# Optimization experiments

Hardware: AMD Instinct MI355X
Metric: run time of the kernel (lower is better)

The kernel has to match this reference:

```python
import jax, jax.numpy as jnp
import numpy as np

N_USER = 500_000
N_GROUP = 100_000
N_EDGE = 5_000_000
DIM = 64
NORM_2 = -1.0  # exponent for back-pass degree norm (module default)
ALPHA = 0.0    # residual mix coefficient (module default)


def setup_inputs() -> dict:
    key = jax.random.key(0)
    k1, k2, k3, k4 = jax.random.split(key, 4)
    h_user = jax.random.normal(k1, (N_USER, DIM), dtype=jnp.float32)
    h_group = jax.random.normal(k2, (N_GROUP, DIM), dtype=jnp.float32)
    edge_src = jax.random.randint(k3, (N_EDGE,), 0, N_USER, dtype=jnp.int64)
    edge_dst = jax.random.randint(k4, (N_EDGE,), 0, N_GROUP, dtype=jnp.int64)
    return {"h_user": h_user, "h_group": h_group,
            "edge_src": edge_src, "edge_dst": edge_dst}


def reference(h_user, h_group, edge_src, edge_dst):
    # Forward pass: copy_src -> sum aggregate onto dst, normalize by in-degree^-1.
    ones = jnp.ones((edge_src.shape[0],), dtype=h_user.dtype)
    deg_dst = jax.ops.segment_sum(ones, edge_dst, num_segments=N_GROUP)
    deg_dst = jnp.maximum(deg_dst, 1.0)  # clamp(min=1)
    rst = jax.ops.segment_sum(h_user[edge_src], edge_dst, num_segments=N_GROUP)
    if ALPHA != 0.0:
        rst = rst + ALPHA * h_group
    rst = rst * (1.0 / deg_dst)[:, None]  # [N_GROUP, DIM]
    # Back pass: aggregate rst back onto src via reversed edges, normalize by deg^norm_2.
    deg_src = jax.ops.segment_sum(ones, edge_src, num_segments=N_USER)
    deg_src = jnp.maximum(deg_src, 1.0)
    bsrc = jax.ops.segment_sum(rst[edge_dst], edge_src, num_segments=N_USER)
    bsrc = bsrc * jnp.power(deg_src, NORM_2)[:, None]  # [N_USER, DIM]
    return bsrc, rst
```

## Files before the change

### kernel.cpp

```cpp
#include <hip/hip_runtime.h>

#define N_USER  500000
#define N_GROUP 100000
#define N_EDGE  5000000
#define DIM     64

#define SCAN_BLOCK 256
#define SCAN_ELEMS 4096
#define PER_THREAD (SCAN_ELEMS / SCAN_BLOCK)

#define KD_SHIFT 7
#define KS_SHIFT 9
#define C_DST ((N_GROUP + (1 << KD_SHIFT) - 1) >> KD_SHIFT)
#define C_SRC ((N_USER  + (1 << KS_SHIFT) - 1) >> KS_SHIFT)
#define TILE_A 16384
#define GRID_A ((N_EDGE + TILE_A - 1) / TILE_A)
#define CVT_BLOCKS 1024
#define CAP_D 7680
#define CAP_S 6272
#define MD_N (C_DST * GRID_A)
#define MS_N (C_SRC * GRID_A)

typedef unsigned int uint32;

__device__ inline unsigned short f2bf(float x) {
    uint32 b = __float_as_uint(x);
    uint32 r = (b + 0x7FFFu + ((b >> 16) & 1u)) >> 16;
    return (unsigned short)r;
}
__device__ inline float ldt(const float* t, size_t i) { return t[i]; }
__device__ inline float ldt(const unsigned short* t, size_t i) {
    return __uint_as_float((uint32)t[i] << 16);
}

__global__ void prep_kernel(const int* __restrict__ src,
                            const int* __restrict__ dst,
                            int* __restrict__ mat_d,
                            int* __restrict__ mat_s,
                            const float* __restrict__ hin,
                            unsigned short* __restrict__ h16) {
    __shared__ int hd[C_DST], hs[C_SRC];
    int tid = threadIdx.x;
    int b = blockIdx.x;
    if (b < GRID_A) {
        long base = (long)b * TILE_A;
        for (int k = tid; k < C_DST; k += blockDim.x) hd[k] = 0;
        for (int k = tid; k < C_SRC; k += blockDim.x) hs[k] = 0;
        __syncthreads();
        for (int i = tid; i < TILE_A; i += blockDim.x) {
            long e = base + i;
            if (e >= N_EDGE) break;
            atomicAdd(&hd[dst[e] >> KD_SHIFT], 1);
            atomicAdd(&hs[src[e] >> KS_SHIFT], 1);
        }
        __syncthreads();
        for (int k = tid; k < C_DST; k += blockDim.x) mat_d[(size_t)k * GRID_A + b] = hd[k];
        for (int k = tid; k < C_SRC; k += blockDim.x) mat_s[(size_t)k * GRID_A + b] = hs[k];
    } else if (h16) {
        long n4 = (long)N_USER * DIM / 4;
        long stride = (long)CVT_BLOCKS * blockDim.x;
        for (long i = (long)(b - GRID_A) * blockDim.x + tid; i < n4; i += stride) {
            const float4 v = ((const float4*)hin)[i];
            ushort4 o;
            o.x = f2bf(v.x); o.y = f2bf(v.y); o.z = f2bf(v.z); o.w = f2bf(v.w);
            ((ushort4*)h16)[i] = o;
        }
    }
}

__global__ void scan1_kernel(const int* __restrict__ cnt,
                             int* __restrict__ off,
                             int* __restrict__ partial,
                             int n) {
    __shared__ int sh[SCAN_BLOCK];
    int tid = threadIdx.x;
    int tbase = blockIdx.x * SCAN_ELEMS + tid * PER_THREAD;
    int local[PER_THREAD];
    int sum = 0;
#pragma unroll
    for (int i = 0; i < PER_THREAD; ++i) {
        int idx = tbase + i;
        int v = (idx < n) ? cnt[idx] : 0;
        local[i] = sum;
        sum += v;
    }
    sh[tid] = sum;
    __syncthreads();
    for (int o = 1; o < SCAN_BLOCK; o <<= 1) {
        int t = (tid >= o) ? sh[tid - o] : 0;
        __syncthreads();
        sh[tid] += t;
        __syncthreads();
    }
    int texc = sh[tid] - sum;
    int blockTotal = sh[SCAN_BLOCK - 1];
#pragma unroll
    for (int i = 0; i < PER_THREAD; ++i) {
        int idx = tbase + i;
        if (idx < n) off[idx] = local[i] + texc;
    }
    if (tid == 0) partial[blockIdx.x] = blockTotal;
}

__global__ void scan2_kernel(int* __restrict__ partial, int nb,
                             int* __restrict__ off_end) {
    __shared__ int sh[SCAN_BLOCK];
    int tid = threadIdx.x;
    int v = (tid < nb) ? partial[tid] : 0;
    sh[tid] = v;
    __syncthreads();
    for (int o = 1; o < SCAN_BLOCK; o <<= 1) {
        int t = (tid >= o) ? sh[tid - o] : 0;
        __syncthreads();
        sh[tid] += t;
        __syncthreads();
    }
    if (tid < nb) partial[tid] = sh[tid] - v;
    if (tid == 0) *off_end = sh[SCAN_BLOCK - 1];
}

__global__ void scan3_kernel(int* __restrict__ off,
                             const int* __restrict__ partial, int n) {
    int base = blockIdx.x * SCAN_ELEMS;
    int add = partial[blockIdx.x];
    for (int i = threadIdx.x; i < SCAN_ELEMS; i += blockDim.x) {
        int idx = base + i;
        if (idx < n) off[idx] += add;
    }
}

__global__ void passA(const int* __restrict__ src,
                      const int* __restrict__ dst,
                      const int* __restrict__ mat_d,
                      const int* __restrict__ mat_s,
                      uint32* __restrict__ coarse_dst,
                      uint32* __restrict__ coarse_src) {
    __shared__ int bd[C_DST], bs[C_SRC];
    int tid = threadIdx.x;
    int b = blockIdx.x;
    long base = (long)b * TILE_A;

    for (int c = tid; c < C_DST; c += blockDim.x) bd[c] = mat_d[(size_t)c * GRID_A + b];
    for (int c = tid; c < C_SRC; c += blockDim.x) bs[c] = mat_s[(size_t)c * GRID_A + b];
    __syncthreads();

    for (int i = tid; i < TILE_A; i += blockDim.x) {
        long e = base + i;
        if (e >= N_EDGE) break;
        int g = dst[e], u = src[e];
        int cd = g >> KD_SHIFT;
        int pd = atomicAdd(&bd[cd], 1);
        coarse_dst[pd] = ((uint32)(g & ((1 << KD_SHIFT) - 1)) << 20) | (uint32)u;
        int cs = u >> KS_SHIFT;
        int ps = atomicAdd(&bs[cs], 1);
        coarse_src[ps] = ((uint32)(u & ((1 << KS_SHIFT) - 1)) << 20) | (uint32)g;
    }
}

template <int SHIFT, int CAP, int U, bool NT, typename T>
__global__ __launch_bounds__(512) void sortgather(
    const uint32* __restrict__ coarse,
    const int* __restrict__ mat,
    const T* __restrict__ table,
    float* __restrict__ out,
    unsigned short* __restrict__ p0,
    unsigned short* __restrict__ p1,
    int n) {
    const int NK = 1 << SHIFT;
    __shared__ int vals[CAP];
    __shared__ int hist[NK];
    __shared__ int cur[NK];
    int tid = threadIdx.x;
    int c = blockIdx.x;
    int lo_g = c << SHIFT;
    int beg = mat[(size_t)c * GRID_A];
    int end = mat[(size_t)(c + 1) * GRID_A];
    int cnt = end - beg;
    int stg = min(cnt, CAP);

    for (int k = tid; k < NK; k += 512) hist[k] = 0;
    __syncthreads();

    for (int i = tid; i < stg; i += 512) {
        atomicAdd(&hist[coarse[beg + i] >> 20], 1);
    }
    __syncthreads();

    for (int o = 1; o < NK; o <<= 1) {
        int t = (tid < NK && tid >= o) ? hist[tid - o] : 0;
        __syncthreads();
        if (tid < NK) hist[tid] += t;
        __syncthreads();
    }
    if (tid < NK) cur[tid] = (tid == 0) ? 0 : hist[tid - 1];
    __syncthreads();

    for (int i = tid; i < stg; i += 512) {
        uint32 kv = coarse[beg + i];
        int p = atomicAdd(&cur[kv >> 20], 1);
        vals[p] = (int)(kv & 0xFFFFFu);
    }
    __syncthreads();

    int wv = tid >> 6, lane = tid & 63;
    for (int r = wv; r < NK; r += 8) {
        int row = lo_g + r;
        if (row >= n) break;
        int lo = (r == 0) ? 0 : hist[r - 1];
        int hi = hist[r];
        float a[U];
#pragma unroll
        for (int j = 0; j < U; ++j) a[j] = 0.0f;
        int e = lo;
        for (; e + U <= hi; e += U) {
#pragma unroll
            for (int j = 0; j < U; ++j) {
                int s = vals[e + j];
                a[j] += ldt(table, (size_t)s * DIM + lane);
            }
        }
        for (; e < hi; ++e) {
            int s = vals[e];
            a[0] += ldt(table, (size_t)s * DIM + lane);
        }
        int deg = hi - lo;
        if (stg < cnt) {
            for (int i = beg + stg; i < end; ++i) {
                uint32 kv = coarse[i];
                if ((int)(kv >> 20) == r) {
                    a[0] += ldt(table, (size_t)(kv & 0xFFFFFu) * DIM + lane);
                    ++deg;
                }
            }
        }
        float acc = 0.0f;
#pragma unroll
        for (int j = 0; j < U; ++j) acc += a[j];
        float rv = acc / fmaxf((float)deg, 1.0f);
        size_t oidx = (size_t)row * DIM + lane;
        if (NT) __builtin_nontemporal_store(rv, &out[oidx]);
        else out[oidx] = rv;
        if (p0) {
            unsigned short bv = f2bf(rv);
            if (lane < 32) p0[(size_t)row * 32 + lane] = bv;
            else           p1[(size_t)row * 32 + (lane - 32)] = bv;
        }
    }
}

template <int SHIFT, int CAP>
__global__ __launch_bounds__(512) void sortgather_bwd(
    const uint32* __restrict__ coarse,
    const int* __restrict__ mat,
    const unsigned short* __restrict__ p0,
    const unsigned short* __restrict__ p1,
    float* __restrict__ out,
    int n) {
    const int NK = 1 << SHIFT;
    __shared__ int vals[CAP];
    __shared__ int hist[NK];
    __shared__ int cur[NK];
    int tid = threadIdx.x;
    int c = blockIdx.x;
    int lo_g = c << SHIFT;
    int beg = mat[(size_t)c * GRID_A];
    int end = mat[(size_t)(c + 1) * GRID_A];
    int cnt = end - beg;
    int stg = min(cnt, CAP);

    for (int k = tid; k < NK; k += 512) hist[k] = 0;
    __syncthreads();
    for (int i = tid; i < stg; i += 512) {
        atomicAdd(&hist[coarse[beg + i] >> 20], 1);
    }
    __syncthreads();
    for (int o = 1; o < NK; o <<= 1) {
        int t = (tid < NK && tid >= o) ? hist[tid - o] : 0;
        __syncthreads();
        if (tid < NK) hist[tid] += t;
        __syncthreads();
    }
    if (tid < NK) cur[tid] = (tid == 0) ? 0 : hist[tid - 1];
    __syncthreads();
    for (int i = tid; i < stg; i += 512) {
        uint32 kv = coarse[beg + i];
        int p = atomicAdd(&cur[kv >> 20], 1);
        vals[p] = (int)(kv & 0xFFFFFu);
    }
    __syncthreads();

    int wv = tid >> 6, lane = tid & 63;
    int sub = lane >> 5, d = lane & 31;
    for (int h = 0; h < 2; ++h) {
        const unsigned short* pl = h ? p1 : p0;
        for (int r = wv; r < NK; r += 8) {
            int row = lo_g + r;
            if (row >= n) break;
            int lo = (r == 0) ? 0 : hist[r - 1];
            int hi = hist[r];
            int deg = hi - lo;
            float a = 0.0f, b2 = 0.0f;
            int e = lo;
            for (; e + 4 <= hi; e += 4) {
                int s0 = vals[e + sub];
                int s1 = vals[e + 2 + sub];
                a  += ldt(pl, (size_t)s0 * 32 + d);
                b2 += ldt(pl, (size_t)s1 * 32 + d);
            }
            for (; e < hi; e += 2) {
                int ee = e + sub;
                float w = (ee < hi) ? 1.0f : 0.0f;
                int s = vals[ee < hi ? ee : hi - 1];
                a += w * ldt(pl, (size_t)s * 32 + d);
            }
            if (stg < cnt) {
                for (int i = beg + stg; i < end; ++i) {
                    uint32 kv = coarse[i];
                    if ((int)(kv >> 20) == r) {
                        float w = (sub == 0) ? 1.0f : 0.0f;
                        a += w * ldt(pl, (size_t)(kv & 0xFFFFFu) * 32 + d);
                        ++deg;
                    }
                }
            }
            float s = a + b2;
            s += __shfl_xor(s, 32);
            float rv = s / fmaxf((float)deg, 1.0f);
            if (sub == 0)
                __builtin_nontemporal_store(rv, &out[(size_t)row * DIM + h * 32 + d]);
        }
    }
}

__global__ void hist_kernel(const int* __restrict__ src,
                            const int* __restrict__ dst,
                            int* __restrict__ cnt_src,
                            int* __restrict__ cnt_dst) {
    int e = blockIdx.x * blockDim.x + threadIdx.x;
    if (e < N_EDGE) {
        atomicAdd(&cnt_src[src[e]], 1);
        atomicAdd(&cnt_dst[dst[e]], 1);
    }
}

__global__ void fill_both(const int* __restrict__ src,
                          const int* __restrict__ dst,
                          const int* __restrict__ off_src,
                          const int* __restrict__ off_dst,
                          int* __restrict__ cur_src,
                          int* __restrict__ cur_dst,
                          int* __restrict__ bucket_src,
                          int* __restrict__ bucket_dst) {
    int e = blockIdx.x * blockDim.x + threadIdx.x;
    if (e < N_EDGE) {
        int u = src[e];
        int g = dst[e];
        int p = atomicAdd(&cur_src[u], 1);
        bucket_src[off_src[u] + p] = g;
        int q = atomicAdd(&cur_dst[g], 1);
        bucket_dst[off_dst[g] + q] = u;
    }
}

__global__ void fill_one(const int* __restrict__ key,
                         const int* __restrict__ val,
                         const int* __restrict__ off,
                         int* __restrict__ cur,
                         int* __restrict__ bucket) {
    int e = blockIdx.x * blockDim.x + threadIdx.x;
    if (e < N_EDGE) {
        int k = key[e];
        int p = atomicAdd(&cur[k], 1);
        bucket[off[k] + p] = val[e];
    }
}

__global__ void cvt_bf16(const float* __restrict__ in,
                         unsigned short* __restrict__ out, long n4) {
    long i = (long)blockIdx.x * blockDim.x + threadIdx.x;
    if (i >= n4) return;
    const float4 v = ((const float4*)in)[i];
    ushort4 o;
    o.x = f2bf(v.x); o.y = f2bf(v.y); o.z = f2bf(v.z); o.w = f2bf(v.w);
    ((ushort4*)out)[i] = o;
}

template <int NROW, bool NT, int U, typename T>
__global__ void gather_kernel(const int* __restrict__ off,
                              const int* __restrict__ bucket,
                              const T* __restrict__ table,
                              float* __restrict__ out,
                              unsigned short* __restrict__ out16) {
    int wid = (blockIdx.x * blockDim.x + threadIdx.x) >> 6;
    int lane = threadIdx.x & 63;
    if (wid >= NROW) return;
    int beg = off[wid], end = off[wid + 1];

    float a[U];
#pragma unroll
    for (int j = 0; j < U; ++j) a[j] = 0.0f;

    for (int b = beg; b < end; b += 64) {
        int navail = min(64, end - b);
        int sv = bucket[b + (lane < navail ? lane : 0)];
        int k = 0;
        for (; k + U <= navail; k += U) {
#pragma unroll
            for (int j = 0; j < U; ++j) {
                int s = __shfl(sv, k + j);
                a[j] += ldt(table, (size_t)s * DIM + lane);
            }
        }
        if (k < navail) {
#pragma unroll
            for (int j = 0; j < U; ++j) {
                int kk = k + j;
                int s = __shfl(sv, kk < navail ? kk : navail - 1);
                float w = (kk < navail) ? 1.0f : 0.0f;
                a[j] += w * ldt(table, (size_t)s * DIM + lane);
            }
        }
    }
    float acc = 0.0f;
#pragma unroll
    for (int j = 0; j < U; ++j) acc += a[j];
    float inv = 1.0f / fmaxf((float)(end - beg), 1.0f);
    float r = acc * inv;
    if (NT) {
        __builtin_nontemporal_store(r, &out[(size_t)wid * DIM + lane]);
    } else {
        out[(size_t)wid * DIM + lane] = r;
    }
    if (out16) out16[(size_t)wid * DIM + lane] = f2bf(r);
}

__global__ void deg_kernel(const int* __restrict__ src,
                           const int* __restrict__ dst,
                           float* __restrict__ deg_src,
                           float* __restrict__ deg_dst) {
    int e = blockIdx.x * blockDim.x + threadIdx.x;
    if (e < N_EDGE) {
        unsafeAtomicAdd(&deg_src[src[e]], 1.0f);
        unsafeAtomicAdd(&deg_dst[dst[e]], 1.0f);
    }
}

__global__ void scatter_fwd(const int* __restrict__ src,
                            const int* __restrict__ dst,
                            const float* __restrict__ h_user,
                            float* __restrict__ rst) {
    long idx = (long)blockIdx.x * blockDim.x + threadIdx.x;
    if (idx >= (long)N_EDGE * DIM) return;
    int e = (int)(idx >> 6), d = (int)(idx & 63);
    unsafeAtomicAdd(&rst[(long)dst[e] * DIM + d], h_user[(long)src[e] * DIM + d]);
}

__global__ void norm_kernel(float* __restrict__ x,
                            const float* __restrict__ deg, long total) {
    long idx = (long)blockIdx.x * blockDim.x + threadIdx.x;
    if (idx >= total) return;
    float dg = fmaxf(deg[idx >> 6], 1.0f);
    x[idx] *= (1.0f / dg);
}

__global__ void scatter_bwd(const int* __restrict__ src,
                            const int* __restrict__ dst,
                            const float* __restrict__ rst,
                            float* __restrict__ bsrc) {
    long idx = (long)blockIdx.x * blockDim.x + threadIdx.x;
    if (idx >= (long)N_EDGE * DIM) return;
    int e = (int)(idx >> 6), d = (int)(idx & 63);
    unsafeAtomicAdd(&bsrc[(long)src[e] * DIM + d], rst[(long)dst[e] * DIM + d]);
}

extern "C" void kernel_launch(void* const* d_in, const int* in_sizes, int n_in,
                              void* d_out, int out_size, void* d_ws, size_t ws_size,
                              hipStream_t stream) {
    const float* h_user   = (const float*)d_in[0];
    const int*   edge_src = (const int*)d_in[2];
    const int*   edge_dst = (const int*)d_in[3];

    float* bsrc = (float*)d_out;
    float* rst  = bsrc + (size_t)N_USER * DIM;

    const int BLK = 256;
    const int grid_e = (N_EDGE + BLK - 1) / BLK;

    int* ws      = (int*)d_ws;
    int* cnt_dst = ws;
    int* off_dst = cnt_dst + N_GROUP;
    int* cnt_src = off_dst + N_GROUP + 1;
    int* off_src = cnt_src + N_USER;
    int* cur_dst = off_src + N_USER + 1;
    int* cur_src = cur_dst + N_GROUP;
    int* partial = cur_src + N_USER;
    int* bucket_dst = partial + 256;
    int* bucket_src = bucket_dst + N_EDGE;
    unsigned short* r16 = (unsigned short*)(bucket_src + N_EDGE);
    unsigned short* h16 = r16 + (size_t)N_GROUP * DIM;
    unsigned short* rp0 = r16;
    unsigned short* rp1 = r16 + (size_t)N_GROUP * 32;
    size_t tail = ((size_t)((char*)(h16 + (size_t)N_USER * DIM) - (char*)d_ws) + 7) & ~(size_t)7;
    int* mat_d = (int*)((char*)d_ws + tail);
    int* mat_s = mat_d + MD_N + 1;
    size_t tail2 = ((size_t)((char*)(mat_s + MS_N + 1) - (char*)d_ws) + 7) & ~(size_t)7;
    uint32* coarse_dst = (uint32*)((char*)d_ws + tail2);
    uint32* coarse_src = coarse_dst + N_EDGE;

    size_t need_csr1 = (size_t)((bucket_dst + N_EDGE) - ws) * sizeof(int);
    size_t need_csr2 = (size_t)((bucket_src + N_EDGE) - ws) * sizeof(int);
    size_t need_r16  = need_csr2 + (size_t)N_GROUP * DIM * 2;
    size_t need_full = need_r16 + (size_t)N_USER * DIM * 2;
    size_t need_ms   = (size_t)((char*)(coarse_src + N_EDGE) - (char*)d_ws);

    int nb_dst = (N_GROUP + SCAN_ELEMS - 1) / SCAN_ELEMS;
    int nb_src = (N_USER + SCAN_ELEMS - 1) / SCAN_ELEMS;

    if (ws_size >= need_ms) {
        bool use_h16 = (ws_size >= need_full);
        bool use_r16 = (ws_size >= need_r16);

        int gridP = GRID_A + (use_h16 ? CVT_BLOCKS : 0);
        prep_kernel<<<gridP, BLK, 0, stream>>>(edge_src, edge_dst, mat_d, mat_s,
                                               h_user, use_h16 ? h16 : nullptr);

        int nb_md = (MD_N + SCAN_ELEMS - 1) / SCAN_ELEMS;
        int nb_ms = (MS_N + SCAN_ELEMS - 1) / SCAN_ELEMS;
        scan1_kernel<<<nb_md, SCAN_BLOCK, 0, stream>>>(mat_d, mat_d, partial, MD_N);
        scan2_kernel<<<1, SCAN_BLOCK, 0, stream>>>(partial, nb_md, mat_d + MD_N);
        scan3_kernel<<<nb_md, SCAN_BLOCK, 0, stream>>>(mat_d, partial, MD_N);
        scan1_kernel<<<nb_ms, SCAN_BLOCK, 0, stream>>>(mat_s, mat_s, partial, MS_N);
        scan2_kernel<<<1, SCAN_BLOCK, 0, stream>>>(partial, nb_ms, mat_s + MS_N);
        scan3_kernel<<<nb_ms, SCAN_BLOCK, 0, stream>>>(mat_s, partial, MS_N);

        passA<<<GRID_A, BLK, 0, stream>>>(edge_src, edge_dst, mat_d, mat_s,
                                          coarse_dst, coarse_src);

        if (use_h16) {
            sortgather<KD_SHIFT, CAP_D, 8, false, unsigned short>
                <<<C_DST, 512, 0, stream>>>(coarse_dst, mat_d, h16, rst,
                                            use_r16 ? rp0 : nullptr,
                                            use_r16 ? rp1 : nullptr, N_GROUP);
        } else {
            sortgather<KD_SHIFT, CAP_D, 8, false, float>
                <<<C_DST, 512, 0, stream>>>(coarse_dst, mat_d, h_user, rst,
                                            use_r16 ? rp0 : nullptr,
                                            use_r16 ? rp1 : nullptr, N_GROUP);
        }
        if (use_r16) {
            sortgather_bwd<KS_SHIFT, CAP_S>
                <<<C_SRC, 512, 0, stream>>>(coarse_src, mat_s, rp0, rp1, bsrc, N_USER);
        } else {
            sortgather<KS_SHIFT, CAP_S, 4, true, float>
                <<<C_SRC, 512, 0, stream>>>(coarse_src, mat_s, rst, bsrc,
                                            nullptr, nullptr, N_USER);
        }
        return;
    }

    if (ws_size >= need_csr2) {
        bool use_h16 = (ws_size >= need_full);
        bool use_r16 = (ws_size >= need_r16);

        hipMemsetAsync(d_ws, 0, (size_t)(partial - ws) * sizeof(int), stream);

        if (use_h16) {
            long n4 = (long)N_USER * DIM / 4;
            cvt_bf16<<<(int)((n4 + BLK - 1) / BLK), BLK, 0, stream>>>(h_user, h16, n4);
        }

        hist_kernel<<<grid_e, BLK, 0, stream>>>(edge_src, edge_dst, cnt_src, cnt_dst);

        scan1_kernel<<<nb_dst, SCAN_BLOCK, 0, stream>>>(cnt_dst, off_dst, partial, N_GROUP);
        scan2_kernel<<<1, SCAN_BLOCK, 0, stream>>>(partial, nb_dst, off_dst + N_GROUP);
        scan3_kernel<<<nb_dst, SCAN_BLOCK, 0, stream>>>(off_dst, partial, N_GROUP);

        scan1_kernel<<<nb_src, SCAN_BLOCK, 0, stream>>>(cnt_src, off_src, partial, N_USER);
        scan2_kernel<<<1, SCAN_BLOCK, 0, stream>>>(partial, nb_src, off_src + N_USER);
        scan3_kernel<<<nb_src, SCAN_BLOCK, 0, stream>>>(off_src, partial, N_USER);

        fill_both<<<grid_e, BLK, 0, stream>>>(
            edge_src, edge_dst, off_src, off_dst,
            cur_src, cur_dst, bucket_src, bucket_dst);

        unsigned short* r16p = use_r16 ? r16 : (unsigned short*)nullptr;
        if (use_h16) {
            gather_kernel<N_GROUP, false, 8, unsigned short>
                <<<(N_GROUP * 64 + BLK - 1) / BLK, BLK, 0, stream>>>(
                    off_dst, bucket_dst, h16, rst, r16p);
        } else {
            gather_kernel<N_GROUP, false, 8, float>
                <<<(N_GROUP * 64 + BLK - 1) / BLK, BLK, 0, stream>>>(
                    off_dst, bucket_dst, h_user, rst, r16p);
        }
        if (use_r16) {
            gather_kernel<N_USER, true, 4, unsigned short>
                <<<(int)(((size_t)N_USER * 64 + BLK - 1) / BLK), BLK, 0, stream>>>(
                    off_src, bucket_src, r16, bsrc, nullptr);
        } else {
            gather_kernel<N_USER, true, 4, float>
                <<<(int)(((size_t)N_USER * 64 + BLK - 1) / BLK), BLK, 0, stream>>>(
                    off_src, bucket_src, rst, bsrc, nullptr);
        }
        return;
    }

    if (ws_size >= need_csr1) {
        hipMemsetAsync(d_ws, 0, (size_t)(partial - ws) * sizeof(int), stream);
        hist_kernel<<<grid_e, BLK, 0, stream>>>(edge_src, edge_dst, cnt_src, cnt_dst);

        scan1_kernel<<<nb_dst, SCAN_BLOCK, 0, stream>>>(cnt_dst, off_dst, partial, N_GROUP);
        scan2_kernel<<<1, SCAN_BLOCK, 0, stream>>>(partial, nb_dst, off_dst + N_GROUP);
        scan3_kernel<<<nb_dst, SCAN_BLOCK, 0, stream>>>(off_dst, partial, N_GROUP);

        scan1_kernel<<<nb_src, SCAN_BLOCK, 0, stream>>>(cnt_src, off_src, partial, N_USER);
        scan2_kernel<<<1, SCAN_BLOCK, 0, stream>>>(partial, nb_src, off_src + N_USER);
        scan3_kernel<<<nb_src, SCAN_BLOCK, 0, stream>>>(off_src, partial, N_USER);

        fill_one<<<grid_e, BLK, 0, stream>>>(edge_dst, edge_src, off_dst, cur_dst, bucket_dst);
        gather_kernel<N_GROUP, false, 8, float>
            <<<(N_GROUP * 64 + BLK - 1) / BLK, BLK, 0, stream>>>(
                off_dst, bucket_dst, h_user, rst, nullptr);

        fill_one<<<grid_e, BLK, 0, stream>>>(edge_src, edge_dst, off_src, cur_src, bucket_dst);
        gather_kernel<N_USER, true, 4, float>
            <<<(int)(((size_t)N_USER * 64 + BLK - 1) / BLK), BLK, 0, stream>>>(
                off_src, bucket_dst, rst, bsrc, nullptr);
        return;
    }

    float* deg_dst = (float*)d_ws;
    float* deg_src = deg_dst + N_GROUP;
    hipMemsetAsync(d_out, 0, (size_t)(N_USER + N_GROUP) * DIM * sizeof(float), stream);
    hipMemsetAsync(d_ws, 0, (size_t)(N_USER + N_GROUP) * sizeof(float), stream);

    deg_kernel<<<grid_e, BLK, 0, stream>>>(edge_src, edge_dst, deg_src, deg_dst);

    long total_ed = (long)N_EDGE * DIM;
    int grid_ed = (int)((total_ed + BLK - 1) / BLK);
    scatter_fwd<<<grid_ed, BLK, 0, stream>>>(edge_src, edge_dst, h_user, rst);
    long total_g = (long)N_GROUP * DIM;
    norm_kernel<<<(int)((total_g + BLK - 1) / BLK), BLK, 0, stream>>>(rst, deg_dst, total_g);
    scatter_bwd<<<grid_ed, BLK, 0, stream>>>(edge_src, edge_dst, rst, bsrc);
    long total_u = (long)N_USER * DIM;
    norm_kernel<<<(int)((total_u + BLK - 1) / BLK), BLK, 0, stream>>>(bsrc, deg_src, total_u);
}
```

Before: 634.6 us.

## Merge dst/src bucket scans into one and drop split-half bf16 backward gather

Lays the dst and src bucket-count matrices out contiguously so a single three-kernel scan produces offsets for both, writing into one shared coarse buffer. This removes three kernel launches. It also stores the bf16 copy of rst as full 64-wide rows instead of two 32-column halves. The backward pass then reuses the generic sortgather kernel (bf16 table, 4-way unroll) in place of the specialized half-row kernel. The change trades the half-split layout's smaller per-pass working set for fewer passes over the edge lists and simpler row gathers.

```diff
diff --git a/kernel.cpp b/kernel.cpp
--- a/kernel.cpp
+++ b/kernel.cpp
@@ -20,6 +20,7 @@
 #define CAP_S 6272
 #define MD_N (C_DST * GRID_A)
 #define MS_N (C_SRC * GRID_A)
+#define MC_N (MD_N + MS_N)
 
 typedef unsigned int uint32;
 
@@ -133,8 +134,7 @@
                       const int* __restrict__ dst,
                       const int* __restrict__ mat_d,
                       const int* __restrict__ mat_s,
-                      uint32* __restrict__ coarse_dst,
-                      uint32* __restrict__ coarse_src) {
+                      uint32* __restrict__ coarse) {
     __shared__ int bd[C_DST], bs[C_SRC];
     int tid = threadIdx.x;
     int b = blockIdx.x;
@@ -150,10 +150,10 @@
         int g = dst[e], u = src[e];
         int cd = g >> KD_SHIFT;
         int pd = atomicAdd(&bd[cd], 1);
-        coarse_dst[pd] = ((uint32)(g & ((1 << KD_SHIFT) - 1)) << 20) | (uint32)u;
+        coarse[pd] = ((uint32)(g & ((1 << KD_SHIFT) - 1)) << 20) | (uint32)u;
         int cs = u >> KS_SHIFT;
         int ps = atomicAdd(&bs[cs], 1);
-        coarse_src[ps] = ((uint32)(u & ((1 << KS_SHIFT) - 1)) << 20) | (uint32)g;
+        coarse[ps] = ((uint32)(u & ((1 << KS_SHIFT) - 1)) << 20) | (uint32)g;
     }
 }
 
@@ -163,8 +163,7 @@
     const int* __restrict__ mat,
     const T* __restrict__ table,
     float* __restrict__ out,
-    unsigned short* __restrict__ p0,
-    unsigned short* __restrict__ p1,
+    unsigned short* __restrict__ out16,
     int n) {
     const int NK = 1 << SHIFT;
     __shared__ int vals[CAP];
@@ -240,95 +239,7 @@
         size_t oidx = (size_t)row * DIM + lane;
         if (NT) __builtin_nontemporal_store(rv, &out[oidx]);
         else out[oidx] = rv;
-        if (p0) {
-            unsigned short bv = f2bf(rv);
-            if (lane < 32) p0[(size_t)row * 32 + lane] = bv;
-            else           p1[(size_t)row * 32 + (lane - 32)] = bv;
-        }
-    }
-}
-
-template <int SHIFT, int CAP>
-__global__ __launch_bounds__(512) void sortgather_bwd(
-    const uint32* __restrict__ coarse,
-    const int* __restrict__ mat,
-    const unsigned short* __restrict__ p0,
-    const unsigned short* __restrict__ p1,
-    float* __restrict__ out,
-    int n) {
-    const int NK = 1 << SHIFT;
-    __shared__ int vals[CAP];
-    __shared__ int hist[NK];
-    __shared__ int cur[NK];
-    int tid = threadIdx.x;
-    int c = blockIdx.x;
-    int lo_g = c << SHIFT;
-    int beg = mat[(size_t)c * GRID_A];
-    int end = mat[(size_t)(c + 1) * GRID_A];
-    int cnt = end - beg;
-    int stg = min(cnt, CAP);
-
-    for (int k = tid; k < NK; k += 512) hist[k] = 0;
-    __syncthreads();
-    for (int i = tid; i < stg; i += 512) {
-        atomicAdd(&hist[coarse[beg + i] >> 20], 1);
-    }
-    __syncthreads();
-    for (int o = 1; o < NK; o <<= 1) {
-        int t = (tid < NK && tid >= o) ? hist[tid - o] : 0;
-        __syncthreads();
-        if (tid < NK) hist[tid] += t;
-        __syncthreads();
-    }
-    if (tid < NK) cur[tid] = (tid == 0) ? 0 : hist[tid - 1];
-    __syncthreads();
-    for (int i = tid; i < stg; i += 512) {
-        uint32 kv = coarse[beg + i];
-        int p = atomicAdd(&cur[kv >> 20], 1);
-        vals[p] = (int)(kv & 0xFFFFFu);
-    }
-    __syncthreads();
-
-    int wv = tid >> 6, lane = tid & 63;
-    int sub = lane >> 5, d = lane & 31;
-    for (int h = 0; h < 2; ++h) {
-        const unsigned short* pl = h ? p1 : p0;
-        for (int r = wv; r < NK; r += 8) {
-            int row = lo_g + r;
-            if (row >= n) break;
-            int lo = (r == 0) ? 0 : hist[r - 1];
-            int hi = hist[r];
-            int deg = hi - lo;
-            float a = 0.0f, b2 = 0.0f;
-            int e = lo;
-            for (; e + 4 <= hi; e += 4) {
-                int s0 = vals[e + sub];
-                int s1 = vals[e + 2 + sub];
-                a  += ldt(pl, (size_t)s0 * 32 + d);
-                b2 += ldt(pl, (size_t)s1 * 32 + d);
-            }
-            for (; e < hi; e += 2) {
-                int ee = e + sub;
-                float w = (ee < hi) ? 1.0f : 0.0f;
-                int s = vals[ee < hi ? ee : hi - 1];
-                a += w * ldt(pl, (size_t)s * 32 + d);
-            }
-            if (stg < cnt) {
-                for (int i = beg + stg; i < end; ++i) {
-                    uint32 kv = coarse[i];
-                    if ((int)(kv >> 20) == r) {
-                        float w = (sub == 0) ? 1.0f : 0.0f;
-                        a += w * ldt(pl, (size_t)(kv & 0xFFFFFu) * 32 + d);
-                        ++deg;
-                    }
-                }
-            }
-            float s = a + b2;
-            s += __shfl_xor(s, 32);
-            float rv = s / fmaxf((float)deg, 1.0f);
-            if (sub == 0)
-                __builtin_nontemporal_store(rv, &out[(size_t)row * DIM + h * 32 + d]);
-        }
+        if (out16) out16[oidx] = f2bf(rv);
     }
 }
 
@@ -498,20 +409,17 @@
     int* bucket_src = bucket_dst + N_EDGE;
     unsigned short* r16 = (unsigned short*)(bucket_src + N_EDGE);
     unsigned short* h16 = r16 + (size_t)N_GROUP * DIM;
-    unsigned short* rp0 = r16;
-    unsigned short* rp1 = r16 + (size_t)N_GROUP * 32;
     size_t tail = ((size_t)((char*)(h16 + (size_t)N_USER * DIM) - (char*)d_ws) + 7) & ~(size_t)7;
     int* mat_d = (int*)((char*)d_ws + tail);
-    int* mat_s = mat_d + MD_N + 1;
+    int* mat_s = mat_d + MD_N;
     size_t tail2 = ((size_t)((char*)(mat_s + MS_N + 1) - (char*)d_ws) + 7) & ~(size_t)7;
-    uint32* coarse_dst = (uint32*)((char*)d_ws + tail2);
-    uint32* coarse_src = coarse_dst + N_EDGE;
+    uint32* coarse = (uint32*)((char*)d_ws + tail2);
 
     size_t need_csr1 = (size_t)((bucket_dst + N_EDGE) - ws) * sizeof(int);
     size_t need_csr2 = (size_t)((bucket_src + N_EDGE) - ws) * sizeof(int);
     size_t need_r16  = need_csr2 + (size_t)N_GROUP * DIM * 2;
     size_t need_full = need_r16 + (size_t)N_USER * DIM * 2;
-    size_t need_ms   = (size_t)((char*)(coarse_src + N_EDGE) - (char*)d_ws);
+    size_t need_ms   = (size_t)((char*)(coarse + 2 * (size_t)N_EDGE) - (char*)d_ws);
 
     int nb_dst = (N_GROUP + SCAN_ELEMS - 1) / SCAN_ELEMS;
     int nb_src = (N_USER + SCAN_ELEMS - 1) / SCAN_ELEMS;
@@ -524,36 +432,27 @@
         prep_kernel<<<gridP, BLK, 0, stream>>>(edge_src, edge_dst, mat_d, mat_s,
                                                h_user, use_h16 ? h16 : nullptr);
 
-        int nb_md = (MD_N + SCAN_ELEMS - 1) / SCAN_ELEMS;
-        int nb_ms = (MS_N + SCAN_ELEMS - 1) / SCAN_ELEMS;
-        scan1_kernel<<<nb_md, SCAN_BLOCK, 0, stream>>>(mat_d, mat_d, partial, MD_N);
-        scan2_kernel<<<1, SCAN_BLOCK, 0, stream>>>(partial, nb_md, mat_d + MD_N);
-        scan3_kernel<<<nb_md, SCAN_BLOCK, 0, stream>>>(mat_d, partial, MD_N);
-        scan1_kernel<<<nb_ms, SCAN_BLOCK, 0, stream>>>(mat_s, mat_s, partial, MS_N);
-        scan2_kernel<<<1, SCAN_BLOCK, 0, stream>>>(partial, nb_ms, mat_s + MS_N);
-        scan3_kernel<<<nb_ms, SCAN_BLOCK, 0, stream>>>(mat_s, partial, MS_N);
-
-        passA<<<GRID_A, BLK, 0, stream>>>(edge_src, edge_dst, mat_d, mat_s,
-                                          coarse_dst, coarse_src);
-
+        int nb_mc = (MC_N + SCAN_ELEMS - 1) / SCAN_ELEMS;
+        scan1_kernel<<<nb_mc, SCAN_BLOCK, 0, stream>>>(mat_d, mat_d, partial, MC_N);
+        scan2_kernel<<<1, SCAN_BLOCK, 0, stream>>>(partial, nb_mc, mat_d + MC_N);
+        scan3_kernel<<<nb_mc, SCAN_BLOCK, 0, stream>>>(mat_d, partial, MC_N);
+
+        passA<<<GRID_A, BLK, 0, stream>>>(edge_src, edge_dst, mat_d, mat_s, coarse);
+
+        unsigned short* r16p = use_r16 ? r16 : (unsigned short*)nullptr;
         if (use_h16) {
             sortgather<KD_SHIFT, CAP_D, 8, false, unsigned short>
-                <<<C_DST, 512, 0, stream>>>(coarse_dst, mat_d, h16, rst,
-                                            use_r16 ? rp0 : nullptr,
-                                            use_r16 ? rp1 : nullptr, N_GROUP);
+                <<<C_DST, 512, 0, stream>>>(coarse, mat_d, h16, rst, r16p, N_GROUP);
         } else {
             sortgather<KD_SHIFT, CAP_D, 8, false, float>
-                <<<C_DST, 512, 0, stream>>>(coarse_dst, mat_d, h_user, rst,
-                                            use_r16 ? rp0 : nullptr,
-                                            use_r16 ? rp1 : nullptr, N_GROUP);
+                <<<C_DST, 512, 0, stream>>>(coarse, mat_d, h_user, rst, r16p, N_GROUP);
         }
         if (use_r16) {
-            sortgather_bwd<KS_SHIFT, CAP_S>
-                <<<C_SRC, 512, 0, stream>>>(coarse_src, mat_s, rp0, rp1, bsrc, N_USER);
+            sortgather<KS_SHIFT, CAP_S, 4, true, unsigned short>
+                <<<C_SRC, 512, 0, stream>>>(coarse, mat_s, r16, bsrc, nullptr, N_USER);
         } else {
             sortgather<KS_SHIFT, CAP_S, 4, true, float>
-                <<<C_SRC, 512, 0, stream>>>(coarse_src, mat_s, rst, bsrc,
-                                            nullptr, nullptr, N_USER);
+                <<<C_SRC, 512, 0, stream>>>(coarse, mat_s, rst, bsrc, nullptr, N_USER);
         }
         return;
     }
```

New measurement: 566.8 us. -10.7%, faster.
